# Performance work log

Measured on AMD Instinct MI355X. Metric: run time of the kernel, lower is better.

The kernel has to match this reference:

```python
import jax, jax.numpy as jnp
import numpy as np

H = 4            # attention heads
C = 128          # hidden_size (per-head channels; concat=False -> mean over heads)
ET = 5           # edge types
IN = 512         # input feature dim
NCLS = 153
N_TOTAL = 100000
N_SRC = (40000, 20000)
N_DST = (30000, 10000)
BATCH = (25000, 8000)
E = (200000, 80000)
EPS = 1e-5


def bn(x, g, b):
    # BatchNorm1d, training-mode batch statistics (biased var), affine
    mu = x.mean(0)
    var = x.var(0)
    return (x - mu) / jnp.sqrt(var + EPS) * g + b


def gat(x_src, src, dst, n_dst, W, att_s, att_d, bias):
    # PyG GATConv, bipartite (x_src, x_src[:n_dst]), shared lin, concat=False
    x = (x_src @ W).reshape(-1, H, C)            # [Ns, H, C]
    a_s = (x * att_s).sum(-1)                    # [Ns, H]
    a_d = (x[:n_dst] * att_d).sum(-1)            # [Nd, H]
    logits = jax.nn.leaky_relu(a_s[src] + a_d[dst], 0.2)   # [E, H]
    m = jax.ops.segment_max(logits, dst, num_segments=n_dst)
    e = jnp.exp(logits - m[dst])
    s = jax.ops.segment_sum(e, dst, num_segments=n_dst)
    coef = e / jnp.maximum(s[dst], 1e-16)        # segment softmax over in-edges
    out = jax.ops.segment_sum(coef[:, :, None] * x[src], dst, num_segments=n_dst)
    return out.mean(1) + bias                    # [Nd, C]


def _layer(feature, li, nodes_idx, src, dst, Ws, bs, bng, bnb, Wg, attS, attD, bg, wp, bp, pg, pb):
    batch, n_dst = BATCH[li], N_DST[li]
    skip = jax.nn.elu(bn(feature @ Ws + bs, bng[0], bnb[0]))
    feats = [skip[:batch]]
    for e2 in range(ET):  # small fixed set of structurally distinct edge types
        xs = feature[nodes_idx[e2]]
        o = gat(xs, src[e2], dst[e2], n_dst, Wg[e2], attS[e2], attD[e2], bg[e2])
        feats.append(jax.nn.elu(bn(o, bng[e2 + 1], bnb[e2 + 1]))[:batch])
    temp = jnp.stack(feats, 1)                   # [batch, ET+1, C]
    attn = jax.nn.softmax(temp @ wp + bp, axis=1)  # [batch, ET+1, 1]
    sk = jnp.einsum('bp,bpc->bc', attn[..., 0], temp)
    return bn(sk, pg, pb)                        # dropout is identity at inference


def setup_inputs():
    key = jax.random.key(0)
    keys = iter(jax.random.split(key, 48))
    def nrm(shape, scale):
        return jax.random.normal(next(keys), shape, dtype=jnp.float32) * scale
    def ri(shape, hi):
        return jax.random.randint(next(keys), shape, 0, hi, dtype=jnp.int32)
    inp = {}
    inp['feature'] = nrm((N_TOTAL, IN), 1.0)
    inp['nodes_idx0'] = ri((ET, N_SRC[0]), N_TOTAL)
    inp['edge_src0'] = ri((ET, E[0]), N_SRC[0])
    inp['edge_dst0'] = jnp.sort(ri((ET, E[0]), N_DST[0]), axis=-1)
    inp['nodes_idx1'] = ri((ET, N_SRC[1]), BATCH[0])
    inp['edge_src1'] = ri((ET, E[1]), N_SRC[1])
    inp['edge_dst1'] = jnp.sort(ri((ET, E[1]), N_DST[1]), axis=-1)
    for l, din in ((0, IN), (1, C)):
        s = str(l)
        sc = 1.0 / float(np.sqrt(din))
        inp['W_skip' + s] = nrm((din, C), sc)
        inp['b_skip' + s] = jnp.zeros((C,), jnp.float32)
        inp['bn_g' + s] = jnp.ones((ET + 1, C), jnp.float32)
        inp['bn_b' + s] = jnp.zeros((ET + 1, C), jnp.float32)
        inp['Wg' + s] = nrm((ET, din, H * C), sc)
        inp['attS' + s] = nrm((ET, H, C), 0.1)
        inp['attD' + s] = nrm((ET, H, C), 0.1)
        inp['bg' + s] = jnp.zeros((ET, C), jnp.float32)
        inp['wp' + s] = nrm((C, 1), 1.0 / float(np.sqrt(C)))
        inp['bp' + s] = jnp.zeros((1,), jnp.float32)
        inp['pg' + s] = jnp.ones((C,), jnp.float32)
        inp['pb' + s] = jnp.zeros((C,), jnp.float32)
    inp['Wm1'] = nrm((C, C), 1.0 / float(np.sqrt(C)))
    inp['bm1'] = jnp.zeros((C,), jnp.float32)
    inp['mg'] = jnp.ones((C,), jnp.float32)
    inp['mb'] = jnp.zeros((C,), jnp.float32)
    inp['Wm2'] = nrm((C, NCLS), 1.0 / float(np.sqrt(C)))
    inp['bm2'] = jnp.zeros((NCLS,), jnp.float32)
    return inp


def reference(feature, nodes_idx0, edge_src0, edge_dst0, nodes_idx1, edge_src1, edge_dst1,
              W_skip0, b_skip0, bn_g0, bn_b0, Wg0, attS0, attD0, bg0, wp0, bp0, pg0, pb0,
              W_skip1, b_skip1, bn_g1, bn_b1, Wg1, attS1, attD1, bg1, wp1, bp1, pg1, pb1,
              Wm1, bm1, mg, mb, Wm2, bm2):
    f = _layer(feature, 0, nodes_idx0, edge_src0, edge_dst0,
               W_skip0, b_skip0, bn_g0, bn_b0, Wg0, attS0, attD0, bg0, wp0, bp0, pg0, pb0)
    f = _layer(f, 1, nodes_idx1, edge_src1, edge_dst1,
               W_skip1, b_skip1, bn_g1, bn_b1, Wg1, attS1, attD1, bg1, wp1, bp1, pg1, pb1)
    h = jax.nn.relu(bn(f @ Wm1 + bm1, mg, mb))
    return h @ Wm2 + bm2
```

## Files before the change

### kernel.cpp

```cpp
#include <hip/hip_runtime.h>
#include <math.h>

#define EPSV 1e-5f
#define NSTATB 960

typedef __attribute__((ext_vector_type(8))) short short8;
typedef __attribute__((ext_vector_type(4))) float floatx4;
typedef _Float16 half2v __attribute__((ext_vector_type(2)));

__device__ __forceinline__ float waveSum(float v) {
#pragma unroll
  for (int off = 32; off > 0; off >>= 1) v += __shfl_xor(v, off, 64);
  return v;
}

__device__ __forceinline__ unsigned bfr(float f) {
  union { float f; unsigned u; } v;
  v.f = f;
  return (v.u + 0x7FFFu + ((v.u >> 16) & 1u)) >> 16;
}

__device__ __forceinline__ void gload16(const short* g, short* l) {
  __builtin_amdgcn_global_load_lds(
      (const __attribute__((address_space(1))) void*)g,
      (__attribute__((address_space(3))) void*)l, 16, 0, 0);
}

__global__ __launch_bounds__(256) void conv_bf16(const float* __restrict__ x,
                                                 short* __restrict__ y, long n4) {
  long i = (long)blockIdx.x * 256 + threadIdx.x;
  long stride = (long)gridDim.x * 256;
  for (; i < n4; i += stride) {
    float4 v = reinterpret_cast<const float4*>(x)[i];
    short4 o;
    o.x = (short)bfr(v.x);
    o.y = (short)bfr(v.y);
    o.z = (short)bfr(v.z);
    o.w = (short)bfr(v.w);
    reinterpret_cast<short4*>(y)[i] = o;
  }
}

__global__ __launch_bounds__(256) void wT_bf16(const float* __restrict__ W0,
                                               short* __restrict__ Wt0, int K, int N,
                                               long wz) {
  const float* W = W0 + (size_t)blockIdx.z * wz;
  short* Wt = Wt0 + (size_t)blockIdx.z * wz;
  __shared__ short t[32][33];
  int k0 = blockIdx.x * 32, n0 = blockIdx.y * 32;
  int x = threadIdx.x & 31, y = threadIdx.x >> 5;
#pragma unroll
  for (int dy = 0; dy < 32; dy += 8) {
    int k = k0 + y + dy, n = n0 + x;
    t[y + dy][x] = (k < K && n < N) ? (short)bfr(W[(size_t)k * N + n]) : (short)0;
  }
  __syncthreads();
#pragma unroll
  for (int dy = 0; dy < 32; dy += 8) {
    int n = n0 + y + dy, k = k0 + x;
    if (n < N && k < K) Wt[(size_t)n * K + k] = t[x][y + dy];
  }
}

__global__ __launch_bounds__(512) void gemm_mfma(
    const short* __restrict__ A, const short* __restrict__ Wt0,
    const float* __restrict__ bias, float* __restrict__ Y0,
    _Float16* __restrict__ Yh0, const int* __restrict__ idx0,
    int M, int K, int N, int mTiles, int nTiles,
    long wtZ, long yZ, int idxZ,
    const float* __restrict__ attS0, const float* __restrict__ attD0,
    float* __restrict__ a_s0, float* __restrict__ a_d0, int n_dst) {
  __shared__ short Alds[3][128 * 32];
  __shared__ short Blds[3][128 * 32];
  __shared__ float sred[128][4];
  int z = blockIdx.z;
  int mt, nt;
  if (nTiles == 1) {
    mt = blockIdx.x;
    nt = 0;
  } else {
    int id = blockIdx.x;
    int slot = id >> 3;
    nt = slot & 3;
    mt = ((slot >> 2) << 3) + (id & 7);
  }
  if (mt >= mTiles) return;
  const short* Wt = Wt0 + (size_t)z * wtZ;
  const int* idx = idx0 ? (idx0 + (size_t)z * idxZ) : nullptr;
  int tid = threadIdx.x;
  int m0 = mt * 128, n0 = nt * 128;

  int srow = tid >> 2, sc = tid & 3;
  int swzc = sc ^ ((srow >> 1) & 3);
  int grow = m0 + srow;
  int ar = (grow < M) ? (idx ? idx[grow] : grow) : 0;
  const short* aSrc = A + (size_t)ar * K + swzc * 8;
  const short* bSrc = Wt + (size_t)(n0 + srow) * K + swzc * 8;
  int wv = tid >> 6, lane = tid & 63;
  int dOff = wv * 512;

  int wm = (wv & 1) * 64, wn = (wv >> 1) * 32;
  int lr = lane & 15, quad = lane >> 4;
  int aoff[4], boff[2];
#pragma unroll
  for (int i = 0; i < 4; i++) {
    int R = wm + i * 16 + lr;
    aoff[i] = R * 32 + ((quad ^ ((R >> 1) & 3)) << 3);
  }
#pragma unroll
  for (int j = 0; j < 2; j++) {
    int R = wn + j * 16 + lr;
    boff[j] = R * 32 + ((quad ^ ((R >> 1) & 3)) << 3);
  }

  floatx4 acc[4][2];
#pragma unroll
  for (int i = 0; i < 4; i++)
#pragma unroll
    for (int j = 0; j < 2; j++) acc[i][j] = (floatx4)0.f;

  auto stage = [&](int slot, int k) {
    gload16(aSrc + k, &Alds[slot][dOff]);
    gload16(bSrc + k, &Blds[slot][dOff]);
  };
  auto compute = [&](int slot) {
    const short* Ab = Alds[slot];
    const short* Bb = Blds[slot];
    short8 af[4], bfv[2];
#pragma unroll
    for (int i = 0; i < 4; i++)
      af[i] = *reinterpret_cast<const short8*>(&Ab[aoff[i]]);
#pragma unroll
    for (int j = 0; j < 2; j++)
      bfv[j] = *reinterpret_cast<const short8*>(&Bb[boff[j]]);
#pragma unroll
    for (int i = 0; i < 4; i++)
#pragma unroll
      for (int j = 0; j < 2; j++)
        acc[i][j] = __builtin_amdgcn_mfma_f32_16x16x32_bf16(af[i], bfv[j],
                                                            acc[i][j], 0, 0, 0);
  };

  stage(0, 0);
  stage(1, 32);
  int NT = K >> 5;
  int cur = 0, nxt = 2;
  for (int t = 0; t < NT; ++t) {
    if (t + 1 < NT) {
      asm volatile("s_waitcnt vmcnt(2)" : : : "memory");
    } else {
      asm volatile("s_waitcnt vmcnt(0)" : : : "memory");
    }
    __builtin_amdgcn_s_barrier();
    __builtin_amdgcn_sched_barrier(0);
    if (t + 2 < NT) stage(nxt, 32 * (t + 2));
    compute(cur);
    cur = (cur == 2) ? 0 : cur + 1;
    nxt = (nxt == 2) ? 0 : nxt + 1;
  }

#pragma unroll
  for (int i = 0; i < 4; i++) {
#pragma unroll
    for (int j = 0; j < 2; j++) {
      int n = n0 + wn + j * 16 + lr;
      float bv = bias ? bias[n] : 0.f;
#pragma unroll
      for (int r = 0; r < 4; r++) {
        int m = m0 + wm + i * 16 + quad * 4 + r;
        if (m < M) {
          float v = acc[i][j][r] + bv;
          if (Yh0) {
            _Float16* Yh = Yh0 + (size_t)z * yZ;
            Yh[(size_t)m * N + n] = (_Float16)v;
          } else {
            float* Y = Y0 + (size_t)z * yZ;
            Y[(size_t)m * N + n] = v;
          }
        }
      }
    }
  }
  if (attS0) {
    int h = nt;
    const float* aSb = attS0 + z * 512 + h * 128;
    const float* aDb = attD0 + z * 512 + h * 128;
    float* asv = a_s0 + (size_t)z * M * 4;
    float* adv = a_d0 + (size_t)z * n_dst * 4;
#pragma unroll
    for (int p = 0; p < 2; p++) {
      const float* av = p ? aDb : aSb;
      float w0a = av[wn + lr], w1a = av[wn + 16 + lr];
#pragma unroll
      for (int i = 0; i < 4; i++) {
#pragma unroll
        for (int r = 0; r < 4; r++) {
          float v = acc[i][0][r] * w0a + acc[i][1][r] * w1a;
          v += __shfl_xor(v, 1, 64);
          v += __shfl_xor(v, 2, 64);
          v += __shfl_xor(v, 4, 64);
          v += __shfl_xor(v, 8, 64);
          if (lr == 0) sred[wm + i * 16 + quad * 4 + r][wv >> 1] = v;
        }
      }
      __syncthreads();
      if (tid < 128) {
        int m = m0 + tid;
        if (m < M) {
          float s = sred[tid][0] + sred[tid][1] + sred[tid][2] + sred[tid][3];
          if (p == 0) asv[(size_t)m * 4 + h] = s;
          else if (m < n_dst) adv[(size_t)m * 4 + h] = s;
        }
      }
      __syncthreads();
    }
  }
}

__global__ __launch_bounds__(256) void gemm_bias(
    const float* __restrict__ A, const float* __restrict__ W,
    const float* __restrict__ bias, float* __restrict__ Y,
    const int* __restrict__ idx, int M, int K, int N) {
  __shared__ float As[16][65];
  __shared__ float Bs[16][64];
  int tid = threadIdx.x;
  int tx = tid & 15, ty = tid >> 4;
  int m0 = blockIdx.x * 64, n0 = blockIdx.y * 64;
  float acc[4][4] = {};
  for (int k0 = 0; k0 < K; k0 += 16) {
    for (int l = tid; l < 64 * 16; l += 256) {
      int r = l >> 4, kk = l & 15;
      int row = m0 + r;
      float v = 0.f;
      if (row < M) {
        int ar = idx ? idx[row] : row;
        v = A[(size_t)ar * K + k0 + kk];
      }
      As[kk][r] = v;
    }
    for (int l = tid; l < 16 * 64; l += 256) {
      int kk = l >> 6, n = l & 63;
      int col = n0 + n;
      Bs[kk][n] = (col < N) ? W[(size_t)(k0 + kk) * N + col] : 0.f;
    }
    __syncthreads();
#pragma unroll
    for (int kk = 0; kk < 16; kk++) {
      float a[4], b[4];
#pragma unroll
      for (int i = 0; i < 4; i++) a[i] = As[kk][ty + 16 * i];
#pragma unroll
      for (int j = 0; j < 4; j++) b[j] = Bs[kk][tx + 16 * j];
#pragma unroll
      for (int i = 0; i < 4; i++)
#pragma unroll
        for (int j = 0; j < 4; j++) acc[i][j] += a[i] * b[j];
    }
    __syncthreads();
  }
#pragma unroll
  for (int i = 0; i < 4; i++) {
    int m = m0 + ty + 16 * i;
    if (m >= M) continue;
#pragma unroll
    for (int j = 0; j < 4; j++) {
      int n = n0 + tx + 16 * j;
      if (n < N) Y[(size_t)m * N + n] = acc[i][j] + (bias ? bias[n] : 0.f);
    }
  }
}

__global__ void build_starts(const int* __restrict__ dst0, int E, int n_dst,
                             int* __restrict__ starts0) {
  const int* dst = dst0 + (size_t)blockIdx.y * E;
  int* starts = starts0 + (size_t)blockIdx.y * (n_dst + 1);
  int k = blockIdx.x * 256 + threadIdx.x;
  if (k > E) return;
  if (k == 0) {
    int d0 = dst[0];
    for (int j = 0; j <= d0; j++) starts[j] = 0;
  } else if (k < E) {
    int d = dst[k], dp = dst[k - 1];
    for (int j = dp + 1; j <= d; j++) starts[j] = k;
  } else {
    int dl = dst[E - 1];
    for (int j = dl + 1; j <= n_dst; j++) starts[j] = E;
  }
}

__global__ void edge_logits(const int* __restrict__ src0, const int* __restrict__ dst0,
                            const float* __restrict__ a_s0, const float* __restrict__ a_d0,
                            float* __restrict__ logits0, int E, int asZ, int adZ) {
  int z = blockIdx.y;
  const int* src = src0 + (size_t)z * E;
  const int* dst = dst0 + (size_t)z * E;
  const float* a_s = a_s0 + (size_t)z * asZ;
  const float* a_d = a_d0 + (size_t)z * adZ;
  float* logits = logits0 + (size_t)z * E * 4;
  int k = blockIdx.x * 256 + threadIdx.x;
  if (k >= E) return;
  int s = src[k], d = dst[k];
#pragma unroll
  for (int h = 0; h < 4; h++) {
    float v = a_s[s * 4 + h] + a_d[d * 4 + h];
    v = (v >= 0.f) ? v : 0.2f * v;
    logits[k * 4 + h] = v;
  }
}

__global__ void node_ms(const float* __restrict__ logits0, const int* __restrict__ starts0,
                        float* __restrict__ ms0, int n_dst, int E) {
  int z = blockIdx.y;
  const float* logits = logits0 + (size_t)z * E * 4;
  const int* starts = starts0 + (size_t)z * (n_dst + 1);
  float* ms = ms0 + (size_t)z * n_dst * 8;
  int t = blockIdx.x * 256 + threadIdx.x;
  int j = t >> 2, h = t & 3;
  if (j >= n_dst) return;
  int r0 = starts[j], r1 = starts[j + 1];
  float m = -1e30f;
  for (int k = r0; k < r1; k++) m = fmaxf(m, logits[k * 4 + h]);
  float s = 0.f;
  for (int k = r0; k < r1; k++) s += __expf(logits[k * 4 + h] - m);
  ms[j * 8 + h] = m;
  ms[j * 8 + 4 + h] = s;
}

__global__ __launch_bounds__(64) void gat_aggregate(
    const _Float16* __restrict__ x0, const float* __restrict__ lg0,
    const int* __restrict__ src0, const int* __restrict__ starts0,
    const float* __restrict__ ms0, const float* __restrict__ bg0,
    float* __restrict__ o0, int n_dst, long xZ, int E) {
  int z = blockIdx.y;
  const _Float16* x = x0 + (size_t)z * xZ;
  const float* lg = lg0 + (size_t)z * E * 4;
  const int* src = src0 + (size_t)z * E;
  const int* starts = starts0 + (size_t)z * (n_dst + 1);
  const float* ms = ms0 + (size_t)z * n_dst * 8;
  const float* bg = bg0 + z * 128;
  float* o = o0 + (size_t)z * (size_t)n_dst * 128;
  int j = blockIdx.x;
  int t = threadIdx.x;
  int r0 = starts[j], r1 = starts[j + 1];
  float m0 = ms[j * 8 + 0], m1 = ms[j * 8 + 1];
  float m2 = ms[j * 8 + 2], m3 = ms[j * 8 + 3];
  float i0 = 1.f / fmaxf(ms[j * 8 + 4], 1e-16f);
  float i1 = 1.f / fmaxf(ms[j * 8 + 5], 1e-16f);
  float i2 = 1.f / fmaxf(ms[j * 8 + 6], 1e-16f);
  float i3 = 1.f / fmaxf(ms[j * 8 + 7], 1e-16f);
  float a00 = 0.f, a01 = 0.f, a10 = 0.f, a11 = 0.f;
  float a20 = 0.f, a21 = 0.f, a30 = 0.f, a31 = 0.f;
  for (int k = r0; k < r1; k++) {
    int s = src[k];
    const half2v* xr = reinterpret_cast<const half2v*>(x + (size_t)s * 512);
    half2v v0 = xr[t];
    half2v v1 = xr[64 + t];
    half2v v2 = xr[128 + t];
    half2v v3 = xr[192 + t];
    float c0 = __expf(lg[k * 4 + 0] - m0) * i0;
    float c1 = __expf(lg[k * 4 + 1] - m1) * i1;
    float c2 = __expf(lg[k * 4 + 2] - m2) * i2;
    float c3 = __expf(lg[k * 4 + 3] - m3) * i3;
    a00 += c0 * (float)v0[0];
    a01 += c0 * (float)v0[1];
    a10 += c1 * (float)v1[0];
    a11 += c1 * (float)v1[1];
    a20 += c2 * (float)v2[0];
    a21 += c2 * (float)v2[1];
    a30 += c3 * (float)v3[0];
    a31 += c3 * (float)v3[1];
  }
  float2 out;
  out.x = 0.25f * (a00 + a10 + a20 + a30) + bg[2 * t];
  out.y = 0.25f * (a01 + a11 + a21 + a31) + bg[2 * t + 1];
  *reinterpret_cast<float2*>(&o[(size_t)j * 128 + 2 * t]) = out;
}

__global__ __launch_bounds__(128) void bn_partial(const float* __restrict__ x0, long xZ,
                                                  float* __restrict__ partial0, int N) {
  const float* x = x0 + (size_t)blockIdx.y * xZ;
  float* partial = partial0 + (size_t)blockIdx.y * (NSTATB * 256);
  int c = threadIdx.x;
  float s = 0.f, ss = 0.f;
  for (int r = blockIdx.x; r < N; r += gridDim.x) {
    float v = x[(size_t)r * 128 + c];
    s += v;
    ss += v * v;
  }
  partial[blockIdx.x * 256 + c] = s;
  partial[blockIdx.x * 256 + 128 + c] = ss;
}

__global__ __launch_bounds__(64) void bn_finalize(const float* __restrict__ partial0,
                                                  int G, int N, float* __restrict__ stats0) {
  const float* partial = partial0 + (size_t)blockIdx.y * (NSTATB * 256);
  float* stats = stats0 + blockIdx.y * 256;
  int c = blockIdx.x;
  int lane = threadIdx.x;
  float s = 0.f, ss = 0.f;
  for (int b = lane; b < G; b += 64) {
    s += partial[b * 256 + c];
    ss += partial[b * 256 + 128 + c];
  }
  s = waveSum(s);
  ss = waveSum(ss);
  if (lane == 0) {
    float mu = s / (float)N;
    float var = ss / (float)N - mu * mu;
    stats[c] = mu;
    stats[128 + c] = rsqrtf(var + EPSV);
  }
}

__global__ __launch_bounds__(128) void bn_apply(
    const float* __restrict__ x0, long xZ, const float* __restrict__ stats0,
    const float* __restrict__ g0, const float* __restrict__ b0, int gz,
    float* __restrict__ y0, short* __restrict__ yb0, long yZ, int M,
    int ostride, int act) {
  int z = blockIdx.y;
  const float* x = x0 + (size_t)z * xZ;
  const float* stats = stats0 + z * 256;
  const float* g = g0 + z * gz;
  const float* b = b0 + z * gz;
  int r = blockIdx.x;
  int c = threadIdx.x;
  if (r >= M) return;
  float v = x[(size_t)r * 128 + c];
  v = (v - stats[c]) * stats[128 + c] * g[c] + b[c];
  if (act == 1) v = (v > 0.f) ? v : (__expf(v) - 1.f);
  if (act == 2) v = fmaxf(v, 0.f);
  if (yb0) {
    short* yb = yb0 + (size_t)z * yZ;
    yb[(size_t)r * ostride + c] = (short)bfr(v);
  } else {
    float* y = y0 + (size_t)z * yZ;
    y[(size_t)r * ostride + c] = v;
  }
}

__global__ __launch_bounds__(128) void pool_attn(
    const float* __restrict__ temp, const float* __restrict__ wp,
    const float* __restrict__ bp, float* __restrict__ sk, int batch) {
  int b = blockIdx.x, c = threadIdx.x;
  int lane = c & 63, wid = c >> 6;
  __shared__ float red[12];
  const float* tr = temp + (size_t)b * 768;
  float wpc = wp[c];
  float t[6];
#pragma unroll
  for (int p = 0; p < 6; p++) t[p] = tr[p * 128 + c];
#pragma unroll
  for (int p = 0; p < 6; p++) {
    float v = waveSum(t[p] * wpc);
    if (lane == 0) red[wid * 6 + p] = v;
  }
  __syncthreads();
  float z[6], m = -1e30f;
#pragma unroll
  for (int p = 0; p < 6; p++) {
    z[p] = red[p] + red[6 + p] + bp[0];
    m = fmaxf(m, z[p]);
  }
  float es = 0.f;
#pragma unroll
  for (int p = 0; p < 6; p++) {
    z[p] = __expf(z[p] - m);
    es += z[p];
  }
  float inv = 1.f / es;
  float o = 0.f;
#pragma unroll
  for (int p = 0; p < 6; p++) o += z[p] * inv * t[p];
  sk[(size_t)b * 128 + c] = o;
}

extern "C" void kernel_launch(void* const* d_in, const int* in_sizes, int n_in,
                              void* d_out, int out_size, void* d_ws, size_t ws_size,
                              hipStream_t stream) {
  const float* feature = (const float*)d_in[0];
  const int* nodes_idx[2] = {(const int*)d_in[1], (const int*)d_in[4]};
  const int* edge_src[2] = {(const int*)d_in[2], (const int*)d_in[5]};
  const int* edge_dst[2] = {(const int*)d_in[3], (const int*)d_in[6]};
  const float *Wsk[2], *bsk[2], *bng[2], *bnb[2], *Wg[2], *attS[2], *attD[2],
      *bg[2], *wp[2], *bp[2], *pg[2], *pb[2];
  for (int l = 0; l < 2; l++) {
    int base = 7 + l * 12;
    Wsk[l] = (const float*)d_in[base + 0];
    bsk[l] = (const float*)d_in[base + 1];
    bng[l] = (const float*)d_in[base + 2];
    bnb[l] = (const float*)d_in[base + 3];
    Wg[l] = (const float*)d_in[base + 4];
    attS[l] = (const float*)d_in[base + 5];
    attD[l] = (const float*)d_in[base + 6];
    bg[l] = (const float*)d_in[base + 7];
    wp[l] = (const float*)d_in[base + 8];
    bp[l] = (const float*)d_in[base + 9];
    pg[l] = (const float*)d_in[base + 10];
    pb[l] = (const float*)d_in[base + 11];
  }
  const float* Wm1 = (const float*)d_in[31];
  const float* bm1 = (const float*)d_in[32];
  const float* mg = (const float*)d_in[33];
  const float* mb = (const float*)d_in[34];
  const float* Wm2 = (const float*)d_in[35];
  const float* bm2 = (const float*)d_in[36];

  float* ws = (float*)d_ws;
  float* bufG5 = ws;   ws += 102400000;
  float* bufSkip = ws; ws += 12800000;
  float* bufO5 = ws;   ws += 19200000;
  float* temp = ws;    ws += 19200000;
  float* f1 = ws;      ws += 1024000;
  float* bufH = ws;    ws += 1024000;
  float* a_s5 = ws;    ws += 800000;
  float* a_d5 = ws;    ws += 600000;
  float* logi5 = ws;   ws += 4000000;
  float* ms5 = ws;     ws += 1200000;
  float* part = ws;    ws += 5 * NSTATB * 256;
  float* stats = ws;   ws += 5 * 256;
  int* starts5 = (int*)ws; ws += 150080;
  short* featB = (short*)ws; ws += 25600000;
  short* f0b = (short*)ws;   ws += 1600000;
  short* wt_sk0 = (short*)ws; ws += 32768;
  short* wt_g0 = (short*)ws;  ws += 655360;
  short* wt_sk1 = (short*)ws; ws += 8192;
  short* wt_g1 = (short*)ws;  ws += 163840;
  _Float16* bufG5h = (_Float16*)bufG5;

  auto cdiv = [](int a, int b) { return (a + b - 1) / b; };

  conv_bf16<<<2048, 256, 0, stream>>>(feature, featB, 100000L * 512 / 4);
  wT_bf16<<<dim3(16, 4, 1), 256, 0, stream>>>(Wsk[0], wt_sk0, 512, 128, 0);
  wT_bf16<<<dim3(16, 16, 5), 256, 0, stream>>>(Wg[0], wt_g0, 512, 512, 512L * 512);
  wT_bf16<<<dim3(4, 4, 1), 256, 0, stream>>>(Wsk[1], wt_sk1, 128, 128, 0);
  wT_bf16<<<dim3(4, 16, 5), 256, 0, stream>>>(Wg[1], wt_g1, 128, 512, 512L * 128);

  auto run_layer = [&](const short* Xb, int Nf, int din, int li, float* fout,
                       short* foutb, const short* wt_sk, const short* wt_g) {
    const int Nsrc = (li == 0) ? 40000 : 20000;
    const int n_dst = (li == 0) ? 30000 : 10000;
    const int batch = (li == 0) ? 25000 : 8000;
    const int E = (li == 0) ? 200000 : 80000;
    const int mtS = cdiv(Nf, 128);
    const int mtG = cdiv(Nsrc, 128);
    const int GpG = cdiv(mtG, 8) * 8;

    gemm_mfma<<<dim3(mtS, 1, 1), 512, 0, stream>>>(
        Xb, wt_sk, bsk[li], bufSkip, nullptr, nullptr, Nf, din, 128, mtS, 1,
        0, 0, 0, nullptr, nullptr, nullptr, nullptr, 0);
    bn_partial<<<dim3(NSTATB, 1), 128, 0, stream>>>(bufSkip, 0, part, Nf);
    bn_finalize<<<dim3(128, 1), 64, 0, stream>>>(part, NSTATB, Nf, stats);
    bn_apply<<<dim3(batch, 1), 128, 0, stream>>>(bufSkip, 0, stats, bng[li],
                                                 bnb[li], 0, temp, nullptr, 0,
                                                 batch, 768, 1);

    gemm_mfma<<<dim3(GpG * 4, 1, 5), 512, 0, stream>>>(
        Xb, wt_g, nullptr, nullptr, bufG5h, nodes_idx[li], Nsrc, din, 512,
        mtG, 4, (long)din * 512, (long)Nsrc * 512, Nsrc,
        attS[li], attD[li], a_s5, a_d5, n_dst);
    build_starts<<<dim3(cdiv(E + 1, 256), 5), 256, 0, stream>>>(edge_dst[li], E,
                                                                n_dst, starts5);
    edge_logits<<<dim3(cdiv(E, 256), 5), 256, 0, stream>>>(
        edge_src[li], edge_dst[li], a_s5, a_d5, logi5, E, Nsrc * 4, n_dst * 4);
    node_ms<<<dim3(cdiv(n_dst * 4, 256), 5), 256, 0, stream>>>(logi5, starts5,
                                                               ms5, n_dst, E);
    gat_aggregate<<<dim3(n_dst, 5), 64, 0, stream>>>(
        bufG5h, logi5, edge_src[li], starts5, ms5, bg[li], bufO5, n_dst,
        (long)Nsrc * 512, E);
    bn_partial<<<dim3(NSTATB, 5), 128, 0, stream>>>(bufO5, (long)n_dst * 128,
                                                    part, n_dst);
    bn_finalize<<<dim3(128, 5), 64, 0, stream>>>(part, NSTATB, n_dst, stats);
    bn_apply<<<dim3(batch, 5), 128, 0, stream>>>(
        bufO5, (long)n_dst * 128, stats, bng[li] + 128, bnb[li] + 128, 128,
        temp + 128, nullptr, 128, batch, 768, 1);

    pool_attn<<<batch, 128, 0, stream>>>(temp, wp[li], bp[li], bufSkip, batch);
    bn_partial<<<dim3(NSTATB, 1), 128, 0, stream>>>(bufSkip, 0, part, batch);
    bn_finalize<<<dim3(128, 1), 64, 0, stream>>>(part, NSTATB, batch, stats);
    bn_apply<<<dim3(batch, 1), 128, 0, stream>>>(bufSkip, 0, stats, pg[li], pb[li],
                                                 0, fout, foutb, 0, batch, 128, 0);
  };

  run_layer(featB, 100000, 512, 0, nullptr, f0b, wt_sk0, wt_g0);
  run_layer(f0b, 25000, 128, 1, f1, nullptr, wt_sk1, wt_g1);

  gemm_bias<<<dim3(cdiv(8000, 64), 2), 256, 0, stream>>>(f1, Wm1, bm1, bufSkip,
                                                         nullptr, 8000, 128, 128);
  bn_partial<<<dim3(NSTATB, 1), 128, 0, stream>>>(bufSkip, 0, part, 8000);
  bn_finalize<<<dim3(128, 1), 64, 0, stream>>>(part, NSTATB, 8000, stats);
  bn_apply<<<8000, 128, 0, stream>>>(bufSkip, 0, stats, mg, mb, 0, bufH,
                                     nullptr, 0, 8000, 128, 2);
  gemm_bias<<<dim3(cdiv(8000, 64), 3), 256, 0, stream>>>(
      bufH, Wm2, bm2, (float*)d_out, nullptr, 8000, 128, 153);
}
```

Measured before the change: 1.301 ms.

## Enlarge MFMA GEMM tile to 256x128 and fuse GAT softmax/aggregation into one kernel

The bf16 MFMA GEMM now uses 256x128 block tiles with each wave computing a 64x64 sub-tile, doubling A staging per step and adjusting the waitcnt and the attention-score reduction. The edge-logit, per-node max/sum and aggregation kernels are merged into one per-destination kernel that recomputes logits from a_s/a_d on the fly, removing the logits and max/sum buffers. The CSR starts construction for both layers is hoisted to the start of the launch sequence. Larger tiles raise register and LDS pressure and reduce block count, and the fused kernel reads a_s three times per edge.

```diff
diff --git a/kernel.cpp b/kernel.cpp
--- a/kernel.cpp
+++ b/kernel.cpp
@@ -62,7 +62,9 @@
   }
 }
 
-__global__ __launch_bounds__(512) void gemm_mfma(
+#define ASZ (256 * 32)
+#define BSZ (128 * 32)
+__global__ __launch_bounds__(512, 4) void gemm_mfma(
     const short* __restrict__ A, const short* __restrict__ Wt0,
     const float* __restrict__ bias, float* __restrict__ Y0,
     _Float16* __restrict__ Yh0, const int* __restrict__ idx0,
@@ -70,9 +72,9 @@
     long wtZ, long yZ, int idxZ,
     const float* __restrict__ attS0, const float* __restrict__ attD0,
     float* __restrict__ a_s0, float* __restrict__ a_d0, int n_dst) {
-  __shared__ short Alds[3][128 * 32];
-  __shared__ short Blds[3][128 * 32];
-  __shared__ float sred[128][4];
+  __shared__ short Alds[3 * ASZ];
+  __shared__ short Blds[3 * BSZ];
+  __shared__ float sred[256][2];
   int z = blockIdx.z;
   int mt, nt;
   if (nTiles == 1) {
@@ -88,55 +90,63 @@
   const short* Wt = Wt0 + (size_t)z * wtZ;
   const int* idx = idx0 ? (idx0 + (size_t)z * idxZ) : nullptr;
   int tid = threadIdx.x;
-  int m0 = mt * 128, n0 = nt * 128;
+  int m0 = mt * 256, n0 = nt * 128;
 
   int srow = tid >> 2, sc = tid & 3;
-  int swzc = sc ^ ((srow >> 1) & 3);
-  int grow = m0 + srow;
-  int ar = (grow < M) ? (idx ? idx[grow] : grow) : 0;
-  const short* aSrc = A + (size_t)ar * K + swzc * 8;
-  const short* bSrc = Wt + (size_t)(n0 + srow) * K + swzc * 8;
+  int rA0 = srow, rA1 = 128 + srow;
+  int swzA0 = sc ^ ((rA0 >> 1) & 3);
+  int swzA1 = sc ^ ((rA1 >> 1) & 3);
+  int swzB = swzA0;
+  int gr0 = m0 + rA0, gr1 = m0 + rA1;
+  int ar0 = (gr0 < M) ? (idx ? idx[gr0] : gr0) : 0;
+  int ar1 = (gr1 < M) ? (idx ? idx[gr1] : gr1) : 0;
+  const short* aSrc0 = A + (size_t)ar0 * K + swzA0 * 8;
+  const short* aSrc1 = A + (size_t)ar1 * K + swzA1 * 8;
+  const short* bSrc = Wt + (size_t)(n0 + srow) * K + swzB * 8;
   int wv = tid >> 6, lane = tid & 63;
-  int dOff = wv * 512;
-
-  int wm = (wv & 1) * 64, wn = (wv >> 1) * 32;
+  int dA0 = wv * 512;
+  int dA1 = 4096 + wv * 512;
+  int dB = wv * 512;
+
+  int wm = (wv & 3) * 64, wn = (wv >> 2) * 64;
   int lr = lane & 15, quad = lane >> 4;
-  int aoff[4], boff[2];
+  int aoff[4], boff[4];
 #pragma unroll
   for (int i = 0; i < 4; i++) {
     int R = wm + i * 16 + lr;
     aoff[i] = R * 32 + ((quad ^ ((R >> 1) & 3)) << 3);
   }
 #pragma unroll
-  for (int j = 0; j < 2; j++) {
+  for (int j = 0; j < 4; j++) {
     int R = wn + j * 16 + lr;
     boff[j] = R * 32 + ((quad ^ ((R >> 1) & 3)) << 3);
   }
 
-  floatx4 acc[4][2];
+  floatx4 acc[4][4];
 #pragma unroll
   for (int i = 0; i < 4; i++)
 #pragma unroll
-    for (int j = 0; j < 2; j++) acc[i][j] = (floatx4)0.f;
+    for (int j = 0; j < 4; j++) acc[i][j] = (floatx4)0.f;
 
   auto stage = [&](int slot, int k) {
-    gload16(aSrc + k, &Alds[slot][dOff]);
-    gload16(bSrc + k, &Blds[slot][dOff]);
+    gload16(aSrc0 + k, &Alds[slot * ASZ + dA0]);
+    gload16(aSrc1 + k, &Alds[slot * ASZ + dA1]);
+    gload16(bSrc + k, &Blds[slot * BSZ + dB]);
   };
   auto compute = [&](int slot) {
-    const short* Ab = Alds[slot];
-    const short* Bb = Blds[slot];
-    short8 af[4], bfv[2];
+    const short* Ab = &Alds[slot * ASZ];
+    const short* Bb = &Blds[slot * BSZ];
+    short8 af[4], bfv[4];
 #pragma unroll
     for (int i = 0; i < 4; i++)
       af[i] = *reinterpret_cast<const short8*>(&Ab[aoff[i]]);
 #pragma unroll
-    for (int j = 0; j < 2; j++)
+    for (int j = 0; j < 4; j++)
       bfv[j] = *reinterpret_cast<const short8*>(&Bb[boff[j]]);
 #pragma unroll
     for (int i = 0; i < 4; i++)
 #pragma unroll
-      for (int j = 0; j < 2; j++)
+      for (int j = 0; j < 4; j++)
         acc[i][j] = __builtin_amdgcn_mfma_f32_16x16x32_bf16(af[i], bfv[j],
                                                             acc[i][j], 0, 0, 0);
   };
@@ -147,7 +157,7 @@
   int cur = 0, nxt = 2;
   for (int t = 0; t < NT; ++t) {
     if (t + 1 < NT) {
-      asm volatile("s_waitcnt vmcnt(2)" : : : "memory");
+      asm volatile("s_waitcnt vmcnt(3)" : : : "memory");
     } else {
       asm volatile("s_waitcnt vmcnt(0)" : : : "memory");
     }
@@ -162,7 +172,7 @@
 #pragma unroll
   for (int i = 0; i < 4; i++) {
 #pragma unroll
-    for (int j = 0; j < 2; j++) {
+    for (int j = 0; j < 4; j++) {
       int n = n0 + wn + j * 16 + lr;
       float bv = bias ? bias[n] : 0.f;
 #pragma unroll
@@ -190,24 +200,27 @@
 #pragma unroll
     for (int p = 0; p < 2; p++) {
       const float* av = p ? aDb : aSb;
-      float w0a = av[wn + lr], w1a = av[wn + 16 + lr];
+      float w[4];
+#pragma unroll
+      for (int j = 0; j < 4; j++) w[j] = av[wn + j * 16 + lr];
 #pragma unroll
       for (int i = 0; i < 4; i++) {
 #pragma unroll
         for (int r = 0; r < 4; r++) {
-          float v = acc[i][0][r] * w0a + acc[i][1][r] * w1a;
+          float v = acc[i][0][r] * w[0] + acc[i][1][r] * w[1] +
+                    acc[i][2][r] * w[2] + acc[i][3][r] * w[3];
           v += __shfl_xor(v, 1, 64);
           v += __shfl_xor(v, 2, 64);
           v += __shfl_xor(v, 4, 64);
           v += __shfl_xor(v, 8, 64);
-          if (lr == 0) sred[wm + i * 16 + quad * 4 + r][wv >> 1] = v;
+          if (lr == 0) sred[wm + i * 16 + quad * 4 + r][wv >> 2] = v;
         }
       }
       __syncthreads();
-      if (tid < 128) {
+      if (tid < 256) {
         int m = m0 + tid;
         if (m < M) {
-          float s = sred[tid][0] + sred[tid][1] + sred[tid][2] + sred[tid][3];
+          float s = sred[tid][0] + sred[tid][1];
           if (p == 0) asv[(size_t)m * 4 + h] = s;
           else if (m < n_dst) adv[(size_t)m * 4 + h] = s;
         }
@@ -288,87 +301,71 @@
   }
 }
 
-__global__ void edge_logits(const int* __restrict__ src0, const int* __restrict__ dst0,
-                            const float* __restrict__ a_s0, const float* __restrict__ a_d0,
-                            float* __restrict__ logits0, int E, int asZ, int adZ) {
+__global__ __launch_bounds__(64) void gat_fused(
+    const _Float16* __restrict__ x0, const float* __restrict__ a_s0,
+    const float* __restrict__ a_d0, const int* __restrict__ src0,
+    const int* __restrict__ starts0, const float* __restrict__ bg0,
+    float* __restrict__ o0, int n_dst, long xZ, int E, int asZ, int adZ) {
   int z = blockIdx.y;
-  const int* src = src0 + (size_t)z * E;
-  const int* dst = dst0 + (size_t)z * E;
+  const _Float16* x = x0 + (size_t)z * xZ;
   const float* a_s = a_s0 + (size_t)z * asZ;
   const float* a_d = a_d0 + (size_t)z * adZ;
-  float* logits = logits0 + (size_t)z * E * 4;
-  int k = blockIdx.x * 256 + threadIdx.x;
-  if (k >= E) return;
-  int s = src[k], d = dst[k];
-#pragma unroll
-  for (int h = 0; h < 4; h++) {
-    float v = a_s[s * 4 + h] + a_d[d * 4 + h];
-    v = (v >= 0.f) ? v : 0.2f * v;
-    logits[k * 4 + h] = v;
-  }
-}
-
-__global__ void node_ms(const float* __restrict__ logits0, const int* __restrict__ starts0,
-                        float* __restrict__ ms0, int n_dst, int E) {
-  int z = blockIdx.y;
-  const float* logits = logits0 + (size_t)z * E * 4;
-  const int* starts = starts0 + (size_t)z * (n_dst + 1);
-  float* ms = ms0 + (size_t)z * n_dst * 8;
-  int t = blockIdx.x * 256 + threadIdx.x;
-  int j = t >> 2, h = t & 3;
-  if (j >= n_dst) return;
-  int r0 = starts[j], r1 = starts[j + 1];
-  float m = -1e30f;
-  for (int k = r0; k < r1; k++) m = fmaxf(m, logits[k * 4 + h]);
-  float s = 0.f;
-  for (int k = r0; k < r1; k++) s += __expf(logits[k * 4 + h] - m);
-  ms[j * 8 + h] = m;
-  ms[j * 8 + 4 + h] = s;
-}
-
-__global__ __launch_bounds__(64) void gat_aggregate(
-    const _Float16* __restrict__ x0, const float* __restrict__ lg0,
-    const int* __restrict__ src0, const int* __restrict__ starts0,
-    const float* __restrict__ ms0, const float* __restrict__ bg0,
-    float* __restrict__ o0, int n_dst, long xZ, int E) {
-  int z = blockIdx.y;
-  const _Float16* x = x0 + (size_t)z * xZ;
-  const float* lg = lg0 + (size_t)z * E * 4;
   const int* src = src0 + (size_t)z * E;
   const int* starts = starts0 + (size_t)z * (n_dst + 1);
-  const float* ms = ms0 + (size_t)z * n_dst * 8;
   const float* bg = bg0 + z * 128;
   float* o = o0 + (size_t)z * (size_t)n_dst * 128;
   int j = blockIdx.x;
   int t = threadIdx.x;
   int r0 = starts[j], r1 = starts[j + 1];
-  float m0 = ms[j * 8 + 0], m1 = ms[j * 8 + 1];
-  float m2 = ms[j * 8 + 2], m3 = ms[j * 8 + 3];
-  float i0 = 1.f / fmaxf(ms[j * 8 + 4], 1e-16f);
-  float i1 = 1.f / fmaxf(ms[j * 8 + 5], 1e-16f);
-  float i2 = 1.f / fmaxf(ms[j * 8 + 6], 1e-16f);
-  float i3 = 1.f / fmaxf(ms[j * 8 + 7], 1e-16f);
+  float4 ad = *reinterpret_cast<const float4*>(&a_d[j * 4]);
+  float m0 = -1e30f, m1 = -1e30f, m2 = -1e30f, m3 = -1e30f;
+  for (int k = r0; k < r1; k++) {
+    int s = src[k];
+    float4 as = *reinterpret_cast<const float4*>(&a_s[s * 4]);
+    float l0 = as.x + ad.x; l0 = (l0 >= 0.f) ? l0 : 0.2f * l0;
+    float l1 = as.y + ad.y; l1 = (l1 >= 0.f) ? l1 : 0.2f * l1;
+    float l2 = as.z + ad.z; l2 = (l2 >= 0.f) ? l2 : 0.2f * l2;
+    float l3 = as.w + ad.w; l3 = (l3 >= 0.f) ? l3 : 0.2f * l3;
+    m0 = fmaxf(m0, l0); m1 = fmaxf(m1, l1);
+    m2 = fmaxf(m2, l2); m3 = fmaxf(m3, l3);
+  }
+  float s0 = 0.f, s1 = 0.f, s2 = 0.f, s3 = 0.f;
+  for (int k = r0; k < r1; k++) {
+    int s = src[k];
+    float4 as = *reinterpret_cast<const float4*>(&a_s[s * 4]);
+    float l0 = as.x + ad.x; l0 = (l0 >= 0.f) ? l0 : 0.2f * l0;
+    float l1 = as.y + ad.y; l1 = (l1 >= 0.f) ? l1 : 0.2f * l1;
+    float l2 = as.z + ad.z; l2 = (l2 >= 0.f) ? l2 : 0.2f * l2;
+    float l3 = as.w + ad.w; l3 = (l3 >= 0.f) ? l3 : 0.2f * l3;
+    s0 += __expf(l0 - m0); s1 += __expf(l1 - m1);
+    s2 += __expf(l2 - m2); s3 += __expf(l3 - m3);
+  }
+  float i0 = 1.f / fmaxf(s0, 1e-16f);
+  float i1 = 1.f / fmaxf(s1, 1e-16f);
+  float i2 = 1.f / fmaxf(s2, 1e-16f);
+  float i3 = 1.f / fmaxf(s3, 1e-16f);
   float a00 = 0.f, a01 = 0.f, a10 = 0.f, a11 = 0.f;
   float a20 = 0.f, a21 = 0.f, a30 = 0.f, a31 = 0.f;
   for (int k = r0; k < r1; k++) {
     int s = src[k];
+    float4 as = *reinterpret_cast<const float4*>(&a_s[s * 4]);
+    float l0 = as.x + ad.x; l0 = (l0 >= 0.f) ? l0 : 0.2f * l0;
+    float l1 = as.y + ad.y; l1 = (l1 >= 0.f) ? l1 : 0.2f * l1;
+    float l2 = as.z + ad.z; l2 = (l2 >= 0.f) ? l2 : 0.2f * l2;
+    float l3 = as.w + ad.w; l3 = (l3 >= 0.f) ? l3 : 0.2f * l3;
+    float c0 = __expf(l0 - m0) * i0;
+    float c1 = __expf(l1 - m1) * i1;
+    float c2 = __expf(l2 - m2) * i2;
+    float c3 = __expf(l3 - m3) * i3;
     const half2v* xr = reinterpret_cast<const half2v*>(x + (size_t)s * 512);
     half2v v0 = xr[t];
     half2v v1 = xr[64 + t];
     half2v v2 = xr[128 + t];
     half2v v3 = xr[192 + t];
-    float c0 = __expf(lg[k * 4 + 0] - m0) * i0;
-    float c1 = __expf(lg[k * 4 + 1] - m1) * i1;
-    float c2 = __expf(lg[k * 4 + 2] - m2) * i2;
-    float c3 = __expf(lg[k * 4 + 3] - m3) * i3;
-    a00 += c0 * (float)v0[0];
-    a01 += c0 * (float)v0[1];
-    a10 += c1 * (float)v1[0];
-    a11 += c1 * (float)v1[1];
-    a20 += c2 * (float)v2[0];
-    a21 += c2 * (float)v2[1];
-    a30 += c3 * (float)v3[0];
-    a31 += c3 * (float)v3[1];
+    a00 += c0 * (float)v0[0]; a01 += c0 * (float)v0[1];
+    a10 += c1 * (float)v1[0]; a11 += c1 * (float)v1[1];
+    a20 += c2 * (float)v2[0]; a21 += c2 * (float)v2[1];
+    a30 += c3 * (float)v3[0]; a31 += c3 * (float)v3[1];
   }
   float2 out;
   out.x = 0.25f * (a00 + a10 + a20 + a30) + bg[2 * t];
@@ -514,11 +511,10 @@
   float* bufH = ws;    ws += 1024000;
   float* a_s5 = ws;    ws += 800000;
   float* a_d5 = ws;    ws += 600000;
-  float* logi5 = ws;   ws += 4000000;
-  float* ms5 = ws;     ws += 1200000;
   float* part = ws;    ws += 5 * NSTATB * 256;
   float* stats = ws;   ws += 5 * 256;
-  int* starts5 = (int*)ws; ws += 150080;
+  int* starts5a = (int*)ws; ws += 150080;
+  int* starts5b = (int*)ws; ws += 50080;
   short* featB = (short*)ws; ws += 25600000;
   short* f0b = (short*)ws;   ws += 1600000;
   short* wt_sk0 = (short*)ws; ws += 32768;
@@ -529,6 +525,10 @@
 
   auto cdiv = [](int a, int b) { return (a + b - 1) / b; };
 
+  build_starts<<<dim3(cdiv(200001, 256), 5), 256, 0, stream>>>(edge_dst[0],
+                                                               200000, 30000, starts5a);
+  build_starts<<<dim3(cdiv(80001, 256), 5), 256, 0, stream>>>(edge_dst[1],
+                                                              80000, 10000, starts5b);
   conv_bf16<<<2048, 256, 0, stream>>>(feature, featB, 100000L * 512 / 4);
   wT_bf16<<<dim3(16, 4, 1), 256, 0, stream>>>(Wsk[0], wt_sk0, 512, 128, 0);
   wT_bf16<<<dim3(16, 16, 5), 256, 0, stream>>>(Wg[0], wt_g0, 512, 512, 512L * 512);
@@ -536,13 +536,14 @@
   wT_bf16<<<dim3(4, 16, 5), 256, 0, stream>>>(Wg[1], wt_g1, 128, 512, 512L * 128);
 
   auto run_layer = [&](const short* Xb, int Nf, int din, int li, float* fout,
-                       short* foutb, const short* wt_sk, const short* wt_g) {
+                       short* foutb, const short* wt_sk, const short* wt_g,
+                       int* starts5) {
     const int Nsrc = (li == 0) ? 40000 : 20000;
     const int n_dst = (li == 0) ? 30000 : 10000;
     const int batch = (li == 0) ? 25000 : 8000;
     const int E = (li == 0) ? 200000 : 80000;
-    const int mtS = cdiv(Nf, 128);
-    const int mtG = cdiv(Nsrc, 128);
+    const int mtS = cdiv(Nf, 256);
+    const int mtG = cdiv(Nsrc, 256);
     const int GpG = cdiv(mtG, 8) * 8;
 
     gemm_mfma<<<dim3(mtS, 1, 1), 512, 0, stream>>>(
@@ -558,15 +559,9 @@
         Xb, wt_g, nullptr, nullptr, bufG5h, nodes_idx[li], Nsrc, din, 512,
         mtG, 4, (long)din * 512, (long)Nsrc * 512, Nsrc,
         attS[li], attD[li], a_s5, a_d5, n_dst);
-    build_starts<<<dim3(cdiv(E + 1, 256), 5), 256, 0, stream>>>(edge_dst[li], E,
-                                                                n_dst, starts5);
-    edge_logits<<<dim3(cdiv(E, 256), 5), 256, 0, stream>>>(
-        edge_src[li], edge_dst[li], a_s5, a_d5, logi5, E, Nsrc * 4, n_dst * 4);
-    node_ms<<<dim3(cdiv(n_dst * 4, 256), 5), 256, 0, stream>>>(logi5, starts5,
-                                                               ms5, n_dst, E);
-    gat_aggregate<<<dim3(n_dst, 5), 64, 0, stream>>>(
-        bufG5h, logi5, edge_src[li], starts5, ms5, bg[li], bufO5, n_dst,
-        (long)Nsrc * 512, E);
+    gat_fused<<<dim3(n_dst, 5), 64, 0, stream>>>(
+        bufG5h, a_s5, a_d5, edge_src[li], starts5, bg[li], bufO5, n_dst,
+        (long)Nsrc * 512, E, Nsrc * 4, n_dst * 4);
     bn_partial<<<dim3(NSTATB, 5), 128, 0, stream>>>(bufO5, (long)n_dst * 128,
                                                     part, n_dst);
     bn_finalize<<<dim3(128, 5), 64, 0, stream>>>(part, NSTATB, n_dst, stats);
@@ -581,8 +576,8 @@
                                                  0, fout, foutb, 0, batch, 128, 0);
   };
 
-  run_layer(featB, 100000, 512, 0, nullptr, f0b, wt_sk0, wt_g0);
-  run_layer(f0b, 25000, 128, 1, f1, nullptr, wt_sk1, wt_g1);
+  run_layer(featB, 100000, 512, 0, nullptr, f0b, wt_sk0, wt_g0, starts5a);
+  run_layer(f0b, 25000, 128, 1, f1, nullptr, wt_sk1, wt_g1, starts5b);
 
   gemm_bias<<<dim3(cdiv(8000, 64), 2), 256, 0, stream>>>(f1, Wm1, bm1, bufSkip,
                                                          nullptr, 8000, 128, 128);
```

Result: slower. 1.385 ms (+6.5%).
